# Performance work log

Hardware: AMD Instinct MI355X
Metric: run time of the kernel (lower is better)

## Reference

```python
import jax, jax.numpy as jnp
import numpy as np

D = 2048      # d_hidden
F = 1408      # d_expert (routed)
E = 8         # n_routed_experts
K = 2         # n_experts_per_token
FS = 2816     # shared expert width = d_expert * n_shared_experts
B, S = 2, 1024


def setup_inputs() -> dict:
    key = jax.random.key(0)
    ks = jax.random.split(key, 9)
    sc = 0.02
    return {
        "x": jax.random.normal(ks[0], (B, S, D), dtype=jnp.float32),
        "Wr": jax.random.normal(ks[1], (E, D), dtype=jnp.float32) * sc,   # router Linear(d_hidden, E).weight
        "Wg": jax.random.normal(ks[2], (E, F, D), dtype=jnp.float32) * sc,  # per-expert W_gate.weight [F,D]
        "Wu": jax.random.normal(ks[3], (E, F, D), dtype=jnp.float32) * sc,  # per-expert W_up.weight
        "Wd": jax.random.normal(ks[4], (E, D, F), dtype=jnp.float32) * sc,  # per-expert W_down.weight [D,F]
        "Wsg": jax.random.normal(ks[5], (FS, D), dtype=jnp.float32) * sc,   # shared expert W_gate
        "Wsu": jax.random.normal(ks[6], (FS, D), dtype=jnp.float32) * sc,   # shared expert W_up
        "Wsd": jax.random.normal(ks[7], (D, FS), dtype=jnp.float32) * sc,   # shared expert W_down
    }


def reference(x, Wr, Wg, Wu, Wd, Wsg, Wsu, Wsd):
    silu = jax.nn.silu

    # Shared expert: SwiGLU FFN over all tokens
    sg = silu(jnp.einsum("bsd,fd->bsf", x, Wsg))
    su = jnp.einsum("bsd,fd->bsf", x, Wsu)
    shared_out = jnp.einsum("bsf,df->bsd", sg * su, Wsd)

    # Gating: softmax over expert logits, then top-k (sum-combine is order-invariant)
    logits = jnp.einsum("bsd,ed->bse", x, Wr)
    scores = jax.nn.softmax(logits, axis=-1)
    topk_scores, topk_idx = jax.lax.top_k(scores, K)            # [B,S,K]
    # Dense combine weights [B,S,E]: topk score where selected, else 0
    w_full = jnp.sum(jax.nn.one_hot(topk_idx, E, dtype=x.dtype) * topk_scores[..., None], axis=-2)

    # Routed experts (dense-over-experts equivalent of sorted grouped-GEMM dispatch)
    g = silu(jnp.einsum("bsd,efd->bsef", x, Wg))                # [B,S,E,F]
    u = jnp.einsum("bsd,efd->bsef", x, Wu)
    out_e = jnp.einsum("bsef,edf->bsed", g * u, Wd)             # [B,S,E,D]
    routed_out = jnp.einsum("bsed,bse->bsd", out_e, w_full)

    return routed_out + shared_out
```

## Files before the change

### kernel.cpp

```cpp
#include <hip/hip_runtime.h>
#include <hip/hip_bf16.h>

#define D_HID 2048
#define F_EXP 1408
#define E_NUM 8
#define FS_SH 2816
#define T_TOK 2048

#define O_WSG 0
#define O_WSU 5767168
#define O_WG  11534336
#define O_WU  34603008
#define O_WSD 57671680
#define O_WD  63438848
#define W_TOT 86507520

#define MAXT 24
#define GU_SH_BLK 176
#define GU_GEMM   440
#define GU_CONV   184
#define DN_SH_BLK 64
#define DN_GRID   256
#define RT_BLK    512
#define WC_BLK    1408

typedef __attribute__((ext_vector_type(8))) short bf16x8;
typedef __attribute__((ext_vector_type(4))) float f32x4;
typedef __attribute__((ext_vector_type(4))) unsigned short u16x4;

#define AS1 __attribute__((address_space(1)))
#define AS3 __attribute__((address_space(3)))

__device__ __forceinline__ unsigned short f2bf(float f){
  unsigned u = __float_as_uint(f);
  u += 0x7fffu + ((u >> 16) & 1u);
  return (unsigned short)(u >> 16);
}
__device__ __forceinline__ float bf2f(unsigned short h){
  return __uint_as_float(((unsigned)h) << 16);
}

__global__ __launch_bounds__(256) void prep_kernel(
    const float* __restrict__ x,  const float* __restrict__ Wr,
    const float* __restrict__ Wsg, const float* __restrict__ Wsu,
    const float* __restrict__ Wg,  const float* __restrict__ Wu,
    unsigned short* __restrict__ xb, unsigned short* __restrict__ wb,
    int* __restrict__ topk_e, float* __restrict__ topk_w)
{
  const int b = blockIdx.x;
  if (b >= RT_BLK){
    const int cb = b - RT_BLK;
    const long nchunk = (long)O_WSD / 8;
    for (long i = (long)cb*256 + threadIdx.x; i < nchunk; i += (long)WC_BLK*256){
      const long e0 = i * 8;
      const float* src; long lo;
      if      (e0 < (long)O_WSU){ src = Wsg; lo = e0; }
      else if (e0 < (long)O_WG ){ src = Wsu; lo = e0 - O_WSU; }
      else if (e0 < (long)O_WU ){ src = Wg;  lo = e0 - O_WG;  }
      else                      { src = Wu;  lo = e0 - O_WU;  }
      const float4 va = ((const float4*)(src + lo))[0];
      const float4 vb = ((const float4*)(src + lo))[1];
      u16x4 h0, h1;
      h0[0]=f2bf(va.x); h0[1]=f2bf(va.y); h0[2]=f2bf(va.z); h0[3]=f2bf(va.w);
      h1[0]=f2bf(vb.x); h1[1]=f2bf(vb.y); h1[2]=f2bf(vb.z); h1[3]=f2bf(vb.w);
      ((u16x4*)(wb + e0))[0] = h0;
      ((u16x4*)(wb + e0))[1] = h1;
    }
    return;
  }
  const int lane = threadIdx.x & 63;
  const int t = b*4 + (threadIdx.x >> 6);
  const float* xt = x + (size_t)t * D_HID;
  unsigned short* xbt = xb + (size_t)t * D_HID;
  float acc[E_NUM];
  #pragma unroll
  for (int e=0;e<E_NUM;e++) acc[e]=0.f;
  #pragma unroll
  for (int j=0;j<8;j++){
    const int d = j*256 + lane*4;
    const float4 v = *(const float4*)(xt + d);
    u16x4 h;
    h[0]=f2bf(v.x); h[1]=f2bf(v.y); h[2]=f2bf(v.z); h[3]=f2bf(v.w);
    *(u16x4*)(xbt + d) = h;
    #pragma unroll
    for (int e=0;e<E_NUM;e++){
      const float4 w = *(const float4*)(Wr + e*D_HID + d);
      acc[e] += v.x*w.x + v.y*w.y + v.z*w.z + v.w*w.w;
    }
  }
  #pragma unroll
  for (int e=0;e<E_NUM;e++){
    #pragma unroll
    for (int off=32; off>0; off>>=1) acc[e] += __shfl_xor(acc[e], off);
  }
  if (lane==0){
    float m = acc[0];
    #pragma unroll
    for (int e=1;e<E_NUM;e++) m = fmaxf(m, acc[e]);
    float p[E_NUM]; float s = 0.f;
    #pragma unroll
    for (int e=0;e<E_NUM;e++){ p[e] = expf(acc[e]-m); s += p[e]; }
    const float inv = 1.f/s;
    int i0=0; float b0=p[0];
    #pragma unroll
    for (int e=1;e<E_NUM;e++) if (p[e] > b0){ b0=p[e]; i0=e; }
    int i1=-1; float b1=-1.f;
    #pragma unroll
    for (int e=0;e<E_NUM;e++) if (e!=i0 && p[e] > b1){ b1=p[e]; i1=e; }
    topk_e[t*2+0]=i0; topk_e[t*2+1]=i1;
    topk_w[t*2+0]=b0*inv; topk_w[t*2+1]=b1*inv;
  }
}

__global__ __launch_bounds__(1024) void build_lists_kernel(
    const int* __restrict__ topk_e, const float* __restrict__ topk_w,
    int* __restrict__ cnt, int* __restrict__ offs,
    int* __restrict__ assign_token, float* __restrict__ assign_w,
    int* __restrict__ token_slot,
    int* __restrict__ tile_rowbase, int* __restrict__ tile_e,
    int* __restrict__ tile_valid, int* __restrict__ n_rt)
{
  const int tid  = threadIdx.x;
  const int lane = tid & 63;
  const int wv   = tid >> 6;
  __shared__ int wsum[E_NUM][16];
  __shared__ int tot_s[E_NUM];
  __shared__ int offs_s[E_NUM];

  int   e_loc[4];
  float w_loc[4];
  #pragma unroll
  for (int j=0;j<4;j++){ e_loc[j]=topk_e[tid*4+j]; w_loc[j]=topk_w[tid*4+j]; }

  int c[E_NUM];
  #pragma unroll
  for (int e=0;e<E_NUM;e++){
    int s = 0;
    #pragma unroll
    for (int j=0;j<4;j++) s += (e_loc[j]==e) ? 1 : 0;
    c[e] = s;
  }
  int pre[E_NUM];
  #pragma unroll
  for (int e=0;e<E_NUM;e++){
    int v = c[e];
    #pragma unroll
    for (int off=1; off<64; off<<=1){
      int t = __shfl_up(v, off);
      if (lane >= off) v += t;
    }
    if (lane==63) wsum[e][wv] = v;
    pre[e] = v - c[e];
  }
  __syncthreads();
  if (tid < E_NUM){
    int s = 0;
    #pragma unroll
    for (int w=0; w<16; w++){ int t = wsum[tid][w]; wsum[tid][w] = s; s += t; }
    tot_s[tid] = s;
    cnt[tid]   = s;
  }
  __syncthreads();
  if (tid == 0){
    int s = 0;
    #pragma unroll
    for (int e=0;e<E_NUM;e++){ offs_s[e] = s; offs[e] = s; s += tot_s[e]; }
    int ntl = 0;
    for (int e=0;e<E_NUM;e++){
      for (int r=0; r<tot_s[e]; r+=256){
        tile_rowbase[ntl] = offs_s[e] + r;
        tile_e[ntl]       = e;
        int v = tot_s[e] - r; if (v > 256) v = 256;
        tile_valid[ntl]   = v;
        ntl++;
      }
    }
    n_rt[0] = ntl;
    for (int i=ntl;i<MAXT;i++){ tile_rowbase[i]=0; tile_e[i]=0; tile_valid[i]=0; }
  }
  __syncthreads();
  int local[E_NUM];
  #pragma unroll
  for (int e=0;e<E_NUM;e++) local[e]=0;
  #pragma unroll
  for (int j=0;j<4;j++){
    const int e = e_loc[j];
    int pos = 0;
    #pragma unroll
    for (int ee=0; ee<E_NUM; ee++)
      if (e == ee) pos = offs_s[ee] + wsum[ee][wv] + pre[ee] + local[ee];
    #pragma unroll
    for (int ee=0; ee<E_NUM; ee++) local[ee] += (e == ee) ? 1 : 0;
    const int entry = tid*4 + j;
    assign_token[pos] = entry >> 1;
    assign_w[pos]     = w_loc[j];
    token_slot[entry] = pos;
  }
}

__global__ __launch_bounds__(512,1) void gateup_fused(
    const unsigned short* __restrict__ xb,
    unsigned short* __restrict__ wb,
    const float* __restrict__ Wsd_f, const float* __restrict__ Wd_f,
    unsigned short* __restrict__ h_shared,
    unsigned short* __restrict__ h_routed,
    const int* __restrict__ tile_rowbase, const int* __restrict__ tile_e,
    const int* __restrict__ tile_valid, const int* __restrict__ n_rt,
    const int* __restrict__ assign_token)
{
  __shared__ __align__(16) char As[4][256*64];
  __shared__ __align__(16) char Bg[4][128*64];
  __shared__ __align__(16) char Bu[4][128*64];

  const int tid  = threadIdx.x;
  const int braw = blockIdx.x;

  if (braw >= GU_GEMM){
    const int cb = braw - GU_GEMM;
    const long nchunk = (long)(W_TOT - O_WSD) / 8;
    for (long i = (long)cb*512 + tid; i < nchunk; i += (long)GU_CONV*512){
      const long e0 = (long)O_WSD + i * 8;
      const float* src; long lo;
      if (e0 < (long)O_WD){ src = Wsd_f; lo = e0 - O_WSD; } else { src = Wd_f; lo = e0 - O_WD; }
      const float4 va = ((const float4*)(src + lo))[0];
      const float4 vb = ((const float4*)(src + lo))[1];
      u16x4 h0, h1;
      h0[0]=f2bf(va.x); h0[1]=f2bf(va.y); h0[2]=f2bf(va.z); h0[3]=f2bf(va.w);
      h1[0]=f2bf(vb.x); h1[1]=f2bf(vb.y); h1[2]=f2bf(vb.z); h1[3]=f2bf(vb.w);
      ((u16x4*)(wb + e0))[0] = h0;
      ((u16x4*)(wb + e0))[1] = h1;
    }
    return;
  }

  const int b = (braw % 8) * (GU_GEMM/8) + braw / 8;

  const int lane = tid & 63;
  const int wave = tid >> 6;
  const int wr = wave >> 1;
  const int wc = wave & 1;

  int nt, rowbase, valid, gather;
  const unsigned short *wg_base, *wu_base;
  unsigned short* H; int N;
  if (b < GU_SH_BLK){
    nt = b >> 3; const int mtile = b & 7;
    rowbase = mtile*256; valid = 256; gather = 0;
    wg_base = wb + O_WSG + (size_t)(nt*128) * D_HID;
    wu_base = wb + O_WSU + (size_t)(nt*128) * D_HID;
    H = h_shared; N = FS_SH;
  } else {
    const int rb = b - GU_SH_BLK;
    const int tile = rb % MAXT;
    nt = rb / MAXT;
    if (tile >= n_rt[0]) return;
    rowbase = tile_rowbase[tile];
    valid   = tile_valid[tile];
    const int e = tile_e[tile];
    gather = 1;
    wg_base = wb + O_WG + ((size_t)e*F_EXP + nt*128) * D_HID;
    wu_base = wb + O_WU + ((size_t)e*F_EXP + nt*128) * D_HID;
    H = h_routed; N = F_EXP;
  }

  f32x4 accg[4][4], accu[4][4];
  const f32x4 z = {0.f,0.f,0.f,0.f};
  #pragma unroll
  for (int m=0;m<4;m++)
    #pragma unroll
    for (int n=0;n<4;n++){ accg[m][n]=z; accu[m][n]=z; }

  const char* asrc[2];
  const int rowmax = rowbase + valid - 1;
  #pragma unroll
  for (int p=0;p<2;p++){
    const int c = p*512 + tid;
    const int row = c >> 2, slot = c & 3;
    const int col16 = slot ^ ((row>>1)&3);
    int idx = rowbase + row;
    if (idx > rowmax) idx = rowmax;
    const size_t grow = gather ? (size_t)assign_token[idx] : (size_t)idx;
    asrc[p] = (const char*)(xb + grow * (size_t)D_HID) + (col16<<4);
  }
  const int brw = tid >> 2, bsl = tid & 3;
  const int bcol16 = bsl ^ ((brw>>1)&3);
  const char* gsrc = (const char*)(wg_base + (size_t)brw * D_HID) + (bcol16<<4);
  const char* usrc = (const char*)(wu_base + (size_t)brw * D_HID) + (bcol16<<4);

  auto stage = [&](int bi, int kt){
    #pragma unroll
    for (int p=0;p<2;p++)
      __builtin_amdgcn_global_load_lds(
        (const AS1 void*)(asrc[p] + kt*64),
        (AS3 void*)(&As[bi][(p*512 + tid)*16]), 16, 0, 0);
    __builtin_amdgcn_global_load_lds(
        (const AS1 void*)(gsrc + kt*64),
        (AS3 void*)(&Bg[bi][tid*16]), 16, 0, 0);
    __builtin_amdgcn_global_load_lds(
        (const AS1 void*)(usrc + kt*64),
        (AS3 void*)(&Bu[bi][tid*16]), 16, 0, 0);
  };

  const int nK = D_HID / 32;
  stage(0,0); stage(1,1); stage(2,2);

  const int arow0 = wr*64 + (lane & 15);
  const int brow0 = wc*64 + (lane & 15);
  const int sread = (lane >> 4) << 4;

  #pragma unroll 1
  for (int kt = 0; kt < nK; ++kt){
    if (kt < nK-2)       asm volatile("s_waitcnt vmcnt(8)\n\ts_barrier" ::: "memory");
    else if (kt == nK-2) asm volatile("s_waitcnt vmcnt(4)\n\ts_barrier" ::: "memory");
    else                 asm volatile("s_waitcnt vmcnt(0)\n\ts_barrier" ::: "memory");
    const int bi = kt & 3;
    bf16x8 a[4], bgr[4], bur[4];
    #pragma unroll
    for (int m=0;m<4;m++){
      const int r = arow0 + m*16;
      a[m] = *(const bf16x8*)(&As[bi][r*64 + (sread ^ (((r>>1)&3)<<4))]);
    }
    #pragma unroll
    for (int n=0;n<4;n++){
      const int r = brow0 + n*16;
      const int ofs = r*64 + (sread ^ (((r>>1)&3)<<4));
      bgr[n] = *(const bf16x8*)(&Bg[bi][ofs]);
      bur[n] = *(const bf16x8*)(&Bu[bi][ofs]);
    }
    if (kt + 3 < nK) stage((kt+3)&3, kt+3);
    #pragma unroll
    for (int m=0;m<4;m++)
      #pragma unroll
      for (int n=0;n<4;n++){
        accg[m][n] = __builtin_amdgcn_mfma_f32_16x16x32_bf16(a[m], bgr[n], accg[m][n], 0,0,0);
        accu[m][n] = __builtin_amdgcn_mfma_f32_16x16x32_bf16(a[m], bur[n], accu[m][n], 0,0,0);
      }
  }

  const int colbase = nt*128 + wc*64;
  #pragma unroll
  for (int m=0;m<4;m++){
    #pragma unroll
    for (int r=0;r<4;r++){
      const int rr = wr*64 + m*16 + ((lane >> 4) << 2) + r;
      if (rr < valid){
        unsigned short* orow = H + (size_t)(rowbase + rr) * N;
        #pragma unroll
        for (int n=0;n<4;n++){
          const int col = colbase + n*16 + (lane & 15);
          const float g2 = accg[m][n][r];
          const float u = accu[m][n][r];
          const float h = (g2 / (1.f + __expf(-g2))) * u;
          orow[col] = f2bf(h);
        }
      }
    }
  }
}

__global__ __launch_bounds__(512,2) void down_fused(
    const unsigned short* __restrict__ h_shared,
    const unsigned short* __restrict__ h_routed,
    const unsigned short* __restrict__ wb,
    float* __restrict__ out, unsigned short* __restrict__ y_routed,
    const int* __restrict__ tile_rowbase, const int* __restrict__ tile_e,
    const int* __restrict__ tile_valid, const int* __restrict__ n_rt)
{
  __shared__ __align__(16) char As[4][256*64];
  __shared__ __align__(16) char Bs[4][256*64];

  const int tid  = threadIdx.x;
  const int braw = blockIdx.x;
  const int b = (braw % 8) * (DN_GRID/8) + braw / 8;
  const int lane = tid & 63;
  const int wave = tid >> 6;
  const int wr = wave >> 1, wc = wave & 1;

  int nt, rowbase, valid, routed, K;
  const unsigned short *A, *w_base;
  if (b < DN_SH_BLK){
    nt = b >> 3; const int mtile = b & 7;
    rowbase = mtile*256; valid = 256; routed = 0;
    A = h_shared; K = FS_SH;
    w_base = wb + O_WSD + (size_t)(nt*256) * FS_SH;
  } else {
    const int rb = b - DN_SH_BLK;
    const int tile = rb % MAXT;
    nt = rb / MAXT;
    if (tile >= n_rt[0]) return;
    rowbase = tile_rowbase[tile];
    valid   = tile_valid[tile];
    const int e = tile_e[tile];
    routed = 1;
    A = h_routed; K = F_EXP;
    w_base = wb + O_WD + ((size_t)e*D_HID + nt*256) * F_EXP;
  }
  const size_t K2 = (size_t)K * 2;

  f32x4 acc[4][8];
  const f32x4 z = {0.f,0.f,0.f,0.f};
  #pragma unroll
  for (int m=0;m<4;m++)
    #pragma unroll
    for (int n=0;n<8;n++) acc[m][n]=z;

  const char* asrc[2];
  const int rowmax = rowbase + valid - 1;
  #pragma unroll
  for (int p=0;p<2;p++){
    const int c = p*512 + tid;
    const int row = c >> 2, slot = c & 3;
    const int col16 = slot ^ ((row>>1)&3);
    int idx = rowbase + row;
    if (idx > rowmax) idx = rowmax;
    asrc[p] = (const char*)A + (size_t)idx * K2 + (col16<<4);
  }
  const char* bsrc[2];
  #pragma unroll
  for (int p=0;p<2;p++){
    const int c = p*512 + tid;
    const int row = c >> 2, slot = c & 3;
    const int col16 = slot ^ ((row>>1)&3);
    bsrc[p] = (const char*)(w_base + (size_t)row * K) + (col16<<4);
  }

  auto stage = [&](int bi, int kt){
    #pragma unroll
    for (int p=0;p<2;p++)
      __builtin_amdgcn_global_load_lds(
        (const AS1 void*)(asrc[p] + kt*64),
        (AS3 void*)(&As[bi][(p*512 + tid)*16]), 16, 0, 0);
    #pragma unroll
    for (int p=0;p<2;p++)
      __builtin_amdgcn_global_load_lds(
        (const AS1 void*)(bsrc[p] + kt*64),
        (AS3 void*)(&Bs[bi][(p*512 + tid)*16]), 16, 0, 0);
  };

  const int nK = K / 32;
  stage(0,0); stage(1,1); stage(2,2);

  const int arow0 = wr*64 + (lane & 15);
  const int brow0 = wc*128 + (lane & 15);
  const int sread = (lane >> 4) << 4;

  #pragma unroll 1
  for (int kt = 0; kt < nK; ++kt){
    if (kt < nK-2)       asm volatile("s_waitcnt vmcnt(8)\n\ts_barrier" ::: "memory");
    else if (kt == nK-2) asm volatile("s_waitcnt vmcnt(4)\n\ts_barrier" ::: "memory");
    else                 asm volatile("s_waitcnt vmcnt(0)\n\ts_barrier" ::: "memory");
    const int bi = kt & 3;
    bf16x8 a[4], bb[8];
    #pragma unroll
    for (int m=0;m<4;m++){
      const int r = arow0 + m*16;
      a[m] = *(const bf16x8*)(&As[bi][r*64 + (sread ^ (((r>>1)&3)<<4))]);
    }
    #pragma unroll
    for (int n=0;n<8;n++){
      const int r = brow0 + n*16;
      bb[n] = *(const bf16x8*)(&Bs[bi][r*64 + (sread ^ (((r>>1)&3)<<4))]);
    }
    if (kt + 3 < nK) stage((kt+3)&3, kt+3);
    #pragma unroll
    for (int m=0;m<4;m++)
      #pragma unroll
      for (int n=0;n<8;n++)
        acc[m][n] = __builtin_amdgcn_mfma_f32_16x16x32_bf16(a[m], bb[n], acc[m][n], 0,0,0);
  }

  const int colbase = nt*256 + wc*128;
  #pragma unroll
  for (int m=0;m<4;m++){
    #pragma unroll
    for (int r=0;r<4;r++){
      const int rr = wr*64 + m*16 + ((lane >> 4) << 2) + r;
      if (rr < valid){
        if (routed){
          unsigned short* orow = y_routed + (size_t)(rowbase + rr) * D_HID;
          #pragma unroll
          for (int n=0;n<8;n++){
            const int col = colbase + n*16 + (lane & 15);
            orow[col] = f2bf(acc[m][n][r]);
          }
        } else {
          float* orow = out + (size_t)(rowbase + rr) * D_HID;
          #pragma unroll
          for (int n=0;n<8;n++){
            const int col = colbase + n*16 + (lane & 15);
            orow[col] = acc[m][n][r];
          }
        }
      }
    }
  }
}

__global__ void combine_kernel(float* __restrict__ out, const unsigned short* __restrict__ y,
                               const int* __restrict__ token_slot,
                               const float* __restrict__ topk_w){
  const int i  = blockIdx.x * blockDim.x + threadIdx.x;
  const int t  = i >> 9;
  const int r4 = i & 511;
  const int s0 = token_slot[t*2+0];
  const int s1 = token_slot[t*2+1];
  const float w0 = topk_w[t*2+0];
  const float w1 = topk_w[t*2+1];
  const u16x4 a = ((const u16x4*)(y + (size_t)s0 * D_HID))[r4];
  const u16x4 bq = ((const u16x4*)(y + (size_t)s1 * D_HID))[r4];
  float4 o = ((float4*)out)[i];
  o.x += w0*bf2f(a[0]) + w1*bf2f(bq[0]);
  o.y += w0*bf2f(a[1]) + w1*bf2f(bq[1]);
  o.z += w0*bf2f(a[2]) + w1*bf2f(bq[2]);
  o.w += w0*bf2f(a[3]) + w1*bf2f(bq[3]);
  ((float4*)out)[i] = o;
}

extern "C" void kernel_launch(void* const* d_in, const int* in_sizes, int n_in,
                              void* d_out, int out_size, void* d_ws, size_t ws_size,
                              hipStream_t stream){
  const float* x   = (const float*)d_in[0];
  const float* Wr  = (const float*)d_in[1];
  const float* Wg  = (const float*)d_in[2];
  const float* Wu  = (const float*)d_in[3];
  const float* Wd  = (const float*)d_in[4];
  const float* Wsg = (const float*)d_in[5];
  const float* Wsu = (const float*)d_in[6];
  const float* Wsd = (const float*)d_in[7];
  float* out = (float*)d_out;
  (void)in_sizes; (void)n_in; (void)out_size; (void)ws_size;

  char* ws = (char*)d_ws;
  size_t off = 0;
  auto alloc = [&](size_t bytes)->char*{
    char* p = ws + off; off += (bytes + 255) & ~(size_t)255; return p;
  };

  unsigned short* wb       = (unsigned short*)alloc((size_t)W_TOT * 2);
  unsigned short* xb       = (unsigned short*)alloc((size_t)T_TOK * D_HID * 2);
  unsigned short* h_shared = (unsigned short*)alloc((size_t)T_TOK * FS_SH * 2);
  unsigned short* h_routed = (unsigned short*)alloc((size_t)T_TOK * 2 * F_EXP * 2);
  unsigned short* y_routed = (unsigned short*)alloc((size_t)T_TOK * 2 * D_HID * 2);
  int*   topk_e       = (int*)alloc(T_TOK*2*sizeof(int));
  float* topk_w       = (float*)alloc(T_TOK*2*sizeof(float));
  int*   cnt          = (int*)alloc(E_NUM*sizeof(int));
  int*   offs         = (int*)alloc(E_NUM*sizeof(int));
  int*   assign_token = (int*)alloc(T_TOK*2*sizeof(int));
  float* assign_w     = (float*)alloc(T_TOK*2*sizeof(float));
  int*   token_slot   = (int*)alloc(T_TOK*2*sizeof(int));
  int*   tile_rowbase = (int*)alloc(MAXT*sizeof(int));
  int*   tile_e       = (int*)alloc(MAXT*sizeof(int));
  int*   tile_valid   = (int*)alloc(MAXT*sizeof(int));
  int*   n_rt         = (int*)alloc(sizeof(int));

  prep_kernel<<<RT_BLK + WC_BLK, 256, 0, stream>>>(
      x, Wr, Wsg, Wsu, Wg, Wu, xb, wb, topk_e, topk_w);
  build_lists_kernel<<<1, 1024, 0, stream>>>(topk_e, topk_w, cnt, offs,
      assign_token, assign_w, token_slot, tile_rowbase, tile_e, tile_valid, n_rt);

  gateup_fused<<<GU_GEMM + GU_CONV, 512, 0, stream>>>(
      xb, wb, Wsd, Wd, h_shared, h_routed, tile_rowbase, tile_e, tile_valid, n_rt, assign_token);
  down_fused<<<DN_GRID, 512, 0, stream>>>(
      h_shared, h_routed, wb, out, y_routed, tile_rowbase, tile_e, tile_valid, n_rt);

  combine_kernel<<<(T_TOK*D_HID/4)/256, 256, 0, stream>>>(out, y_routed, token_slot, topk_w);
}
```

Measured before the change: 326.8 us.

## Double-buffer gate/up GEMM for two blocks per CU and widen weight conversion

The gate/up GEMM drops from a 4-deep LDS ring to a 2-buffer ping-pong, halving shared memory. Launch bounds are raised so two 512-thread blocks can share a CU, with an extra barrier per k-step to guard the buffer swap. Separately, the prep-kernel weight conversion now handles 16 floats per thread instead of 8. The costs are shallower prefetch, more barriers, and tighter register limits. With 128 accumulator values per thread, that limit could force spills.

```diff
diff --git a/kernel.cpp b/kernel.cpp
--- a/kernel.cpp
+++ b/kernel.cpp
@@ -50,21 +50,27 @@
   const int b = blockIdx.x;
   if (b >= RT_BLK){
     const int cb = b - RT_BLK;
-    const long nchunk = (long)O_WSD / 8;
+    const long nchunk = (long)O_WSD / 16;
     for (long i = (long)cb*256 + threadIdx.x; i < nchunk; i += (long)WC_BLK*256){
-      const long e0 = i * 8;
+      const long e0 = i * 16;
       const float* src; long lo;
       if      (e0 < (long)O_WSU){ src = Wsg; lo = e0; }
       else if (e0 < (long)O_WG ){ src = Wsu; lo = e0 - O_WSU; }
       else if (e0 < (long)O_WU ){ src = Wg;  lo = e0 - O_WG;  }
       else                      { src = Wu;  lo = e0 - O_WU;  }
-      const float4 va = ((const float4*)(src + lo))[0];
-      const float4 vb = ((const float4*)(src + lo))[1];
-      u16x4 h0, h1;
-      h0[0]=f2bf(va.x); h0[1]=f2bf(va.y); h0[2]=f2bf(va.z); h0[3]=f2bf(va.w);
-      h1[0]=f2bf(vb.x); h1[1]=f2bf(vb.y); h1[2]=f2bf(vb.z); h1[3]=f2bf(vb.w);
+      const float4 v0 = ((const float4*)(src + lo))[0];
+      const float4 v1 = ((const float4*)(src + lo))[1];
+      const float4 v2 = ((const float4*)(src + lo))[2];
+      const float4 v3 = ((const float4*)(src + lo))[3];
+      u16x4 h0, h1, h2, h3;
+      h0[0]=f2bf(v0.x); h0[1]=f2bf(v0.y); h0[2]=f2bf(v0.z); h0[3]=f2bf(v0.w);
+      h1[0]=f2bf(v1.x); h1[1]=f2bf(v1.y); h1[2]=f2bf(v1.z); h1[3]=f2bf(v1.w);
+      h2[0]=f2bf(v2.x); h2[1]=f2bf(v2.y); h2[2]=f2bf(v2.z); h2[3]=f2bf(v2.w);
+      h3[0]=f2bf(v3.x); h3[1]=f2bf(v3.y); h3[2]=f2bf(v3.z); h3[3]=f2bf(v3.w);
       ((u16x4*)(wb + e0))[0] = h0;
       ((u16x4*)(wb + e0))[1] = h1;
+      ((u16x4*)(wb + e0))[2] = h2;
+      ((u16x4*)(wb + e0))[3] = h3;
     }
     return;
   }
@@ -198,7 +204,7 @@
   }
 }
 
-__global__ __launch_bounds__(512,1) void gateup_fused(
+__global__ __launch_bounds__(512,2) void gateup_fused(
     const unsigned short* __restrict__ xb,
     unsigned short* __restrict__ wb,
     const float* __restrict__ Wsd_f, const float* __restrict__ Wd_f,
@@ -208,9 +214,9 @@
     const int* __restrict__ tile_valid, const int* __restrict__ n_rt,
     const int* __restrict__ assign_token)
 {
-  __shared__ __align__(16) char As[4][256*64];
-  __shared__ __align__(16) char Bg[4][128*64];
-  __shared__ __align__(16) char Bu[4][128*64];
+  __shared__ __align__(16) char As[2][256*64];
+  __shared__ __align__(16) char Bg[2][128*64];
+  __shared__ __align__(16) char Bu[2][128*64];
 
   const int tid  = threadIdx.x;
   const int braw = blockIdx.x;
@@ -301,33 +307,34 @@
         (AS3 void*)(&Bu[bi][tid*16]), 16, 0, 0);
   };
 
-  const int nK = D_HID / 32;
-  stage(0,0); stage(1,1); stage(2,2);
-
   const int arow0 = wr*64 + (lane & 15);
   const int brow0 = wc*64 + (lane & 15);
   const int sread = (lane >> 4) << 4;
 
+  const int nK = D_HID / 32;
+  stage(0, 0);
+  int cur = 0;
   #pragma unroll 1
   for (int kt = 0; kt < nK; ++kt){
-    if (kt < nK-2)       asm volatile("s_waitcnt vmcnt(8)\n\ts_barrier" ::: "memory");
-    else if (kt == nK-2) asm volatile("s_waitcnt vmcnt(4)\n\ts_barrier" ::: "memory");
-    else                 asm volatile("s_waitcnt vmcnt(0)\n\ts_barrier" ::: "memory");
-    const int bi = kt & 3;
+    if (kt + 1 < nK){
+      stage(cur^1, kt+1);
+      asm volatile("s_waitcnt vmcnt(4)\n\ts_barrier" ::: "memory");
+    } else {
+      asm volatile("s_waitcnt vmcnt(0)\n\ts_barrier" ::: "memory");
+    }
     bf16x8 a[4], bgr[4], bur[4];
     #pragma unroll
     for (int m=0;m<4;m++){
       const int r = arow0 + m*16;
-      a[m] = *(const bf16x8*)(&As[bi][r*64 + (sread ^ (((r>>1)&3)<<4))]);
+      a[m] = *(const bf16x8*)(&As[cur][r*64 + (sread ^ (((r>>1)&3)<<4))]);
     }
     #pragma unroll
     for (int n=0;n<4;n++){
       const int r = brow0 + n*16;
       const int ofs = r*64 + (sread ^ (((r>>1)&3)<<4));
-      bgr[n] = *(const bf16x8*)(&Bg[bi][ofs]);
-      bur[n] = *(const bf16x8*)(&Bu[bi][ofs]);
-    }
-    if (kt + 3 < nK) stage((kt+3)&3, kt+3);
+      bgr[n] = *(const bf16x8*)(&Bg[cur][ofs]);
+      bur[n] = *(const bf16x8*)(&Bu[cur][ofs]);
+    }
     #pragma unroll
     for (int m=0;m<4;m++)
       #pragma unroll
@@ -335,6 +342,8 @@
         accg[m][n] = __builtin_amdgcn_mfma_f32_16x16x32_bf16(a[m], bgr[n], accg[m][n], 0,0,0);
         accu[m][n] = __builtin_amdgcn_mfma_f32_16x16x32_bf16(a[m], bur[n], accu[m][n], 0,0,0);
       }
+    asm volatile("s_barrier" ::: "memory");
+    cur ^= 1;
   }
 
   const int colbase = nt*128 + wc*64;
```

Result: slower. 348.9 us (+6.8%).

## Convert gate-up kernel to persistent grid with atomic work queue

Applied to the files above, without the earlier changes.

The gate/up GEMM kernel becomes a persistent kernel of 256 blocks that pull work items from a global atomic counter, which build_lists resets. Items interleave weight-conversion chunks evenly among the shared and routed GEMM tiles. Only the routed tiles that actually exist are enumerated, so idle blocks that used to exit early are gone. This is meant to cut wave quantization and tail imbalance across the CUs. In exchange it adds an atomic and two barriers per item, and it loses the earlier block-index swizzle that grouped tiles for L2 reuse.

```diff
diff --git a/kernel.cpp b/kernel.cpp
--- a/kernel.cpp
+++ b/kernel.cpp
@@ -16,9 +16,9 @@
 #define W_TOT 86507520
 
 #define MAXT 24
-#define GU_SH_BLK 176
-#define GU_GEMM   440
-#define GU_CONV   184
+#define GU_SH_TILE 176
+#define GU_GRID   256
+#define GU_CONVCH 256
 #define DN_SH_BLK 64
 #define DN_GRID   256
 #define RT_BLK    512
@@ -118,7 +118,8 @@
     int* __restrict__ assign_token, float* __restrict__ assign_w,
     int* __restrict__ token_slot,
     int* __restrict__ tile_rowbase, int* __restrict__ tile_e,
-    int* __restrict__ tile_valid, int* __restrict__ n_rt)
+    int* __restrict__ tile_valid, int* __restrict__ n_rt,
+    int* __restrict__ work_ctr)
 {
   const int tid  = threadIdx.x;
   const int lane = tid & 63;
@@ -177,6 +178,7 @@
     }
     n_rt[0] = ntl;
     for (int i=ntl;i<MAXT;i++){ tile_rowbase[i]=0; tile_e[i]=0; tile_valid[i]=0; }
+    work_ctr[0] = 0;
   }
   __syncthreads();
   int local[E_NUM];
@@ -206,152 +208,164 @@
     unsigned short* __restrict__ h_routed,
     const int* __restrict__ tile_rowbase, const int* __restrict__ tile_e,
     const int* __restrict__ tile_valid, const int* __restrict__ n_rt,
-    const int* __restrict__ assign_token)
+    const int* __restrict__ assign_token,
+    int* __restrict__ work_ctr)
 {
   __shared__ __align__(16) char As[4][256*64];
   __shared__ __align__(16) char Bg[4][128*64];
   __shared__ __align__(16) char Bu[4][128*64];
+  __shared__ int item_s;
 
   const int tid  = threadIdx.x;
-  const int braw = blockIdx.x;
-
-  if (braw >= GU_GEMM){
-    const int cb = braw - GU_GEMM;
-    const long nchunk = (long)(W_TOT - O_WSD) / 8;
-    for (long i = (long)cb*512 + tid; i < nchunk; i += (long)GU_CONV*512){
-      const long e0 = (long)O_WSD + i * 8;
-      const float* src; long lo;
-      if (e0 < (long)O_WD){ src = Wsd_f; lo = e0 - O_WSD; } else { src = Wd_f; lo = e0 - O_WD; }
-      const float4 va = ((const float4*)(src + lo))[0];
-      const float4 vb = ((const float4*)(src + lo))[1];
-      u16x4 h0, h1;
-      h0[0]=f2bf(va.x); h0[1]=f2bf(va.y); h0[2]=f2bf(va.z); h0[3]=f2bf(va.w);
-      h1[0]=f2bf(vb.x); h1[1]=f2bf(vb.y); h1[2]=f2bf(vb.z); h1[3]=f2bf(vb.w);
-      ((u16x4*)(wb + e0))[0] = h0;
-      ((u16x4*)(wb + e0))[1] = h1;
-    }
-    return;
-  }
-
-  const int b = (braw % 8) * (GU_GEMM/8) + braw / 8;
-
   const int lane = tid & 63;
   const int wave = tid >> 6;
   const int wr = wave >> 1;
   const int wc = wave & 1;
 
-  int nt, rowbase, valid, gather;
-  const unsigned short *wg_base, *wu_base;
-  unsigned short* H; int N;
-  if (b < GU_SH_BLK){
-    nt = b >> 3; const int mtile = b & 7;
-    rowbase = mtile*256; valid = 256; gather = 0;
-    wg_base = wb + O_WSG + (size_t)(nt*128) * D_HID;
-    wu_base = wb + O_WSU + (size_t)(nt*128) * D_HID;
-    H = h_shared; N = FS_SH;
-  } else {
-    const int rb = b - GU_SH_BLK;
-    const int tile = rb % MAXT;
-    nt = rb / MAXT;
-    if (tile >= n_rt[0]) return;
-    rowbase = tile_rowbase[tile];
-    valid   = tile_valid[tile];
-    const int e = tile_e[tile];
-    gather = 1;
-    wg_base = wb + O_WG + ((size_t)e*F_EXP + nt*128) * D_HID;
-    wu_base = wb + O_WU + ((size_t)e*F_EXP + nt*128) * D_HID;
-    H = h_routed; N = F_EXP;
-  }
-
-  f32x4 accg[4][4], accu[4][4];
-  const f32x4 z = {0.f,0.f,0.f,0.f};
-  #pragma unroll
-  for (int m=0;m<4;m++)
-    #pragma unroll
-    for (int n=0;n<4;n++){ accg[m][n]=z; accu[m][n]=z; }
-
-  const char* asrc[2];
-  const int rowmax = rowbase + valid - 1;
-  #pragma unroll
-  for (int p=0;p<2;p++){
-    const int c = p*512 + tid;
-    const int row = c >> 2, slot = c & 3;
-    const int col16 = slot ^ ((row>>1)&3);
-    int idx = rowbase + row;
-    if (idx > rowmax) idx = rowmax;
-    const size_t grow = gather ? (size_t)assign_token[idx] : (size_t)idx;
-    asrc[p] = (const char*)(xb + grow * (size_t)D_HID) + (col16<<4);
-  }
-  const int brw = tid >> 2, bsl = tid & 3;
-  const int bcol16 = bsl ^ ((brw>>1)&3);
-  const char* gsrc = (const char*)(wg_base + (size_t)brw * D_HID) + (bcol16<<4);
-  const char* usrc = (const char*)(wu_base + (size_t)brw * D_HID) + (bcol16<<4);
-
-  auto stage = [&](int bi, int kt){
-    #pragma unroll
-    for (int p=0;p<2;p++)
-      __builtin_amdgcn_global_load_lds(
-        (const AS1 void*)(asrc[p] + kt*64),
-        (AS3 void*)(&As[bi][(p*512 + tid)*16]), 16, 0, 0);
-    __builtin_amdgcn_global_load_lds(
-        (const AS1 void*)(gsrc + kt*64),
-        (AS3 void*)(&Bg[bi][tid*16]), 16, 0, 0);
-    __builtin_amdgcn_global_load_lds(
-        (const AS1 void*)(usrc + kt*64),
-        (AS3 void*)(&Bu[bi][tid*16]), 16, 0, 0);
-  };
-
-  const int nK = D_HID / 32;
-  stage(0,0); stage(1,1); stage(2,2);
+  const int nrt = n_rt[0];
+  const int ng  = GU_SH_TILE + nrt*11;
+  const int TOT = ng + GU_CONVCH;
 
   const int arow0 = wr*64 + (lane & 15);
   const int brow0 = wc*64 + (lane & 15);
   const int sread = (lane >> 4) << 4;
 
-  #pragma unroll 1
-  for (int kt = 0; kt < nK; ++kt){
-    if (kt < nK-2)       asm volatile("s_waitcnt vmcnt(8)\n\ts_barrier" ::: "memory");
-    else if (kt == nK-2) asm volatile("s_waitcnt vmcnt(4)\n\ts_barrier" ::: "memory");
-    else                 asm volatile("s_waitcnt vmcnt(0)\n\ts_barrier" ::: "memory");
-    const int bi = kt & 3;
-    bf16x8 a[4], bgr[4], bur[4];
-    #pragma unroll
-    for (int m=0;m<4;m++){
-      const int r = arow0 + m*16;
-      a[m] = *(const bf16x8*)(&As[bi][r*64 + (sread ^ (((r>>1)&3)<<4))]);
-    }
-    #pragma unroll
-    for (int n=0;n<4;n++){
-      const int r = brow0 + n*16;
-      const int ofs = r*64 + (sread ^ (((r>>1)&3)<<4));
-      bgr[n] = *(const bf16x8*)(&Bg[bi][ofs]);
-      bur[n] = *(const bf16x8*)(&Bu[bi][ofs]);
-    }
-    if (kt + 3 < nK) stage((kt+3)&3, kt+3);
+  for(;;){
+    __syncthreads();
+    if (tid == 0) item_s = atomicAdd(work_ctr, 1);
+    __syncthreads();
+    const int it = item_s;
+    if (it >= TOT) return;
+
+    const int cbefore = (int)(((long)it * GU_CONVCH) / TOT);
+    const bool isconv = (int)(((long)(it+1) * GU_CONVCH) / TOT) > cbefore;
+    if (isconv){
+      const int cidx = cbefore;
+      const long nchunk = (long)(W_TOT - O_WSD) / 8;
+      for (long j = (long)cidx*512 + tid; j < nchunk; j += (long)GU_CONVCH*512){
+        const long e0 = (long)O_WSD + j * 8;
+        const float* src; long lo;
+        if (e0 < (long)O_WD){ src = Wsd_f; lo = e0 - O_WSD; } else { src = Wd_f; lo = e0 - O_WD; }
+        const float4 va = ((const float4*)(src + lo))[0];
+        const float4 vb = ((const float4*)(src + lo))[1];
+        u16x4 h0, h1;
+        h0[0]=f2bf(va.x); h0[1]=f2bf(va.y); h0[2]=f2bf(va.z); h0[3]=f2bf(va.w);
+        h1[0]=f2bf(vb.x); h1[1]=f2bf(vb.y); h1[2]=f2bf(vb.z); h1[3]=f2bf(vb.w);
+        ((u16x4*)(wb + e0))[0] = h0;
+        ((u16x4*)(wb + e0))[1] = h1;
+      }
+      continue;
+    }
+    const int g = it - cbefore;
+
+    int nt, rowbase, valid, gather;
+    const unsigned short *wg_base, *wu_base;
+    unsigned short* H; int N;
+    if (g < GU_SH_TILE){
+      nt = g >> 3; const int mtile = g & 7;
+      rowbase = mtile*256; valid = 256; gather = 0;
+      wg_base = wb + O_WSG + (size_t)(nt*128) * D_HID;
+      wu_base = wb + O_WSU + (size_t)(nt*128) * D_HID;
+      H = h_shared; N = FS_SH;
+    } else {
+      const int rb = g - GU_SH_TILE;
+      const int tile = rb % nrt;
+      nt = rb / nrt;
+      rowbase = tile_rowbase[tile];
+      valid   = tile_valid[tile];
+      const int e = tile_e[tile];
+      gather = 1;
+      wg_base = wb + O_WG + ((size_t)e*F_EXP + nt*128) * D_HID;
+      wu_base = wb + O_WU + ((size_t)e*F_EXP + nt*128) * D_HID;
+      H = h_routed; N = F_EXP;
+    }
+
+    f32x4 accg[4][4], accu[4][4];
+    const f32x4 z = {0.f,0.f,0.f,0.f};
     #pragma unroll
     for (int m=0;m<4;m++)
       #pragma unroll
+      for (int n=0;n<4;n++){ accg[m][n]=z; accu[m][n]=z; }
+
+    const char* asrc[2];
+    const int rowmax = rowbase + valid - 1;
+    #pragma unroll
+    for (int p=0;p<2;p++){
+      const int c = p*512 + tid;
+      const int row = c >> 2, slot = c & 3;
+      const int col16 = slot ^ ((row>>1)&3);
+      int idx = rowbase + row;
+      if (idx > rowmax) idx = rowmax;
+      const size_t grow = gather ? (size_t)assign_token[idx] : (size_t)idx;
+      asrc[p] = (const char*)(xb + grow * (size_t)D_HID) + (col16<<4);
+    }
+    const int brw = tid >> 2, bsl = tid & 3;
+    const int bcol16 = bsl ^ ((brw>>1)&3);
+    const char* gsrc = (const char*)(wg_base + (size_t)brw * D_HID) + (bcol16<<4);
+    const char* usrc = (const char*)(wu_base + (size_t)brw * D_HID) + (bcol16<<4);
+
+    auto stage = [&](int bi, int kt){
+      #pragma unroll
+      for (int p=0;p<2;p++)
+        __builtin_amdgcn_global_load_lds(
+          (const AS1 void*)(asrc[p] + kt*64),
+          (AS3 void*)(&As[bi][(p*512 + tid)*16]), 16, 0, 0);
+      __builtin_amdgcn_global_load_lds(
+          (const AS1 void*)(gsrc + kt*64),
+          (AS3 void*)(&Bg[bi][tid*16]), 16, 0, 0);
+      __builtin_amdgcn_global_load_lds(
+          (const AS1 void*)(usrc + kt*64),
+          (AS3 void*)(&Bu[bi][tid*16]), 16, 0, 0);
+    };
+
+    const int nK = D_HID / 32;
+    stage(0,0); stage(1,1); stage(2,2);
+
+    #pragma unroll 1
+    for (int kt = 0; kt < nK; ++kt){
+      if (kt < nK-2)       asm volatile("s_waitcnt vmcnt(8)\n\ts_barrier" ::: "memory");
+      else if (kt == nK-2) asm volatile("s_waitcnt vmcnt(4)\n\ts_barrier" ::: "memory");
+      else                 asm volatile("s_waitcnt vmcnt(0)\n\ts_barrier" ::: "memory");
+      const int bi = kt & 3;
+      bf16x8 a[4], bgr[4], bur[4];
+      #pragma unroll
+      for (int m=0;m<4;m++){
+        const int r = arow0 + m*16;
+        a[m] = *(const bf16x8*)(&As[bi][r*64 + (sread ^ (((r>>1)&3)<<4))]);
+      }
+      #pragma unroll
       for (int n=0;n<4;n++){
-        accg[m][n] = __builtin_amdgcn_mfma_f32_16x16x32_bf16(a[m], bgr[n], accg[m][n], 0,0,0);
-        accu[m][n] = __builtin_amdgcn_mfma_f32_16x16x32_bf16(a[m], bur[n], accu[m][n], 0,0,0);
+        const int r = brow0 + n*16;
+        const int ofs = r*64 + (sread ^ (((r>>1)&3)<<4));
+        bgr[n] = *(const bf16x8*)(&Bg[bi][ofs]);
+        bur[n] = *(const bf16x8*)(&Bu[bi][ofs]);
       }
-  }
-
-  const int colbase = nt*128 + wc*64;
-  #pragma unroll
-  for (int m=0;m<4;m++){
-    #pragma unroll
-    for (int r=0;r<4;r++){
-      const int rr = wr*64 + m*16 + ((lane >> 4) << 2) + r;
-      if (rr < valid){
-        unsigned short* orow = H + (size_t)(rowbase + rr) * N;
+      if (kt + 3 < nK) stage((kt+3)&3, kt+3);
+      #pragma unroll
+      for (int m=0;m<4;m++)
         #pragma unroll
         for (int n=0;n<4;n++){
-          const int col = colbase + n*16 + (lane & 15);
-          const float g2 = accg[m][n][r];
-          const float u = accu[m][n][r];
-          const float h = (g2 / (1.f + __expf(-g2))) * u;
-          orow[col] = f2bf(h);
+          accg[m][n] = __builtin_amdgcn_mfma_f32_16x16x32_bf16(a[m], bgr[n], accg[m][n], 0,0,0);
+          accu[m][n] = __builtin_amdgcn_mfma_f32_16x16x32_bf16(a[m], bur[n], accu[m][n], 0,0,0);
+        }
+    }
+
+    const int colbase = nt*128 + wc*64;
+    #pragma unroll
+    for (int m=0;m<4;m++){
+      #pragma unroll
+      for (int r=0;r<4;r++){
+        const int rr = wr*64 + m*16 + ((lane >> 4) << 2) + r;
+        if (rr < valid){
+          unsigned short* orow = H + (size_t)(rowbase + rr) * N;
+          #pragma unroll
+          for (int n=0;n<4;n++){
+            const int col = colbase + n*16 + (lane & 15);
+            const float g2 = accg[m][n][r];
+            const float u = accu[m][n][r];
+            const float h = (g2 / (1.f + __expf(-g2))) * u;
+            orow[col] = f2bf(h);
+          }
         }
       }
     }
@@ -552,14 +566,16 @@
   int*   tile_e       = (int*)alloc(MAXT*sizeof(int));
   int*   tile_valid   = (int*)alloc(MAXT*sizeof(int));
   int*   n_rt         = (int*)alloc(sizeof(int));
+  int*   work_ctr     = (int*)alloc(sizeof(int));
 
   prep_kernel<<<RT_BLK + WC_BLK, 256, 0, stream>>>(
       x, Wr, Wsg, Wsu, Wg, Wu, xb, wb, topk_e, topk_w);
   build_lists_kernel<<<1, 1024, 0, stream>>>(topk_e, topk_w, cnt, offs,
-      assign_token, assign_w, token_slot, tile_rowbase, tile_e, tile_valid, n_rt);
-
-  gateup_fused<<<GU_GEMM + GU_CONV, 512, 0, stream>>>(
-      xb, wb, Wsd, Wd, h_shared, h_routed, tile_rowbase, tile_e, tile_valid, n_rt, assign_token);
+      assign_token, assign_w, token_slot, tile_rowbase, tile_e, tile_valid, n_rt, work_ctr);
+
+  gateup_fused<<<GU_GRID, 512, 0, stream>>>(
+      xb, wb, Wsd, Wd, h_shared, h_routed, tile_rowbase, tile_e, tile_valid, n_rt,
+      assign_token, work_ctr);
   down_fused<<<DN_GRID, 512, 0, stream>>>(
       h_shared, h_routed, wb, out, y_routed, tile_rowbase, tile_e, tile_valid, n_rt);
 
```

New measurement: 335.8 us. 1.03x slower.
